# Kernel tuning notes

Hardware: AMD Instinct MI355X
Metric: run time of the kernel (lower is better)

## Reference

```python
import jax, jax.numpy as jnp
import numpy as np

B, N, SD = 2, 128, 3
IN, H, BD, O, L, WF = 16, 128, 32, 12, 2, 4
DEGREE = 2
EPS = 1e-6


def fibonacci_lattice(n, offset=0.5):
    i = jnp.arange(n, dtype=jnp.float32)
    theta = (jnp.pi * i * (1.0 + np.sqrt(5.0))) % (2.0 * jnp.pi)
    phi = jnp.arccos(1.0 - 2.0 * (i + offset) / (n - 1 + 2 * offset))
    return jnp.stack((jnp.sin(phi) * jnp.cos(theta),
                      jnp.sin(phi) * jnp.sin(theta),
                      jnp.cos(phi)), axis=-1)  # (O, 3)


def poly_features(x, degree=DEGREE):
    feats = [x]
    for _ in range(degree):
        new = jnp.einsum('...i,...j->...ij', feats[-1], x).reshape(x.shape[:-1] + (-1,))
        feats.append(new)
    return jnp.concatenate(feats, axis=-1)


def layernorm(x, scale, bias):
    m = x.mean(axis=-1, keepdims=True)
    v = ((x - m) ** 2).mean(axis=-1, keepdims=True)
    return (x - m) * jax.lax.rsqrt(v + EPS) * scale + bias


def _dense(k, fin, fout):
    return jax.random.normal(k, (fin, fout), jnp.float32) / np.sqrt(fin)


def setup_inputs() -> dict:
    key = jax.random.key(0)
    ks = jax.random.split(key, 32)
    SP_IN = 2 + 4 + 8   # poly features of 2-dim spatial invariants, degree 2
    RO_IN = 1 + 1 + 1   # poly features of 1-dim orientation invariant
    inp = {
        'pos': jax.random.normal(ks[0], (B, N, SD), jnp.float32),
        'x': jax.random.normal(ks[1], (B, N, IN), jnp.float32),
        'mask': jnp.ones((B, N), jnp.float32),
        # spatial kernel basis MLP
        'W1s': _dense(ks[2], SP_IN, H), 'b1s': jnp.zeros((H,), jnp.float32),
        'W2s': _dense(ks[3], H, BD),    'b2s': jnp.zeros((BD,), jnp.float32),
        # rotation kernel basis MLP
        'W1r': _dense(ks[4], RO_IN, H), 'b1r': jnp.zeros((H,), jnp.float32),
        'W2r': _dense(ks[5], H, BD),    'b2r': jnp.zeros((BD,), jnp.float32),
        # x embedder (no bias)
        'We': _dense(ks[6], IN, H),
        # per-layer params, stacked along leading layer axis L
        'Wsp':  jax.random.normal(ks[7], (L, BD, H), jnp.float32) / np.sqrt(BD),
        'Wrot': jax.random.normal(ks[8], (L, BD, H), jnp.float32) / np.sqrt(BD),
        'conv_b': jnp.zeros((L, H), jnp.float32),
        'ln_scale': jnp.ones((L, H), jnp.float32),
        'ln_bias': jnp.zeros((L, H), jnp.float32),
        'Wl1': jax.random.normal(ks[9], (L, H, WF * H), jnp.float32) / np.sqrt(H),
        'bl1': jnp.zeros((L, WF * H), jnp.float32),
        'Wl2': jax.random.normal(ks[10], (L, WF * H, H), jnp.float32) / np.sqrt(WF * H),
        'bl2': jnp.zeros((L, H), jnp.float32),
        # readout
        'Wro': _dense(ks[11], H, 1), 'bro': jnp.zeros((1,), jnp.float32),
    }
    return inp


def reference(pos, x, mask, W1s, b1s, W2s, b2s, W1r, b1r, W2r, b2r, We,
              Wsp, Wrot, conv_b, ln_scale, ln_bias, Wl1, bl1, Wl2, bl2, Wro, bro):
    ori = fibonacci_lattice(O)                                   # (O, 3)
    # pairwise relative positions: (B, N_dst=m? note: original indexing)
    rel_pos = pos[:, None, :, None, :] - pos[:, :, None, None, :]  # (B,N,N,1,3)
    inv1 = (rel_pos * ori[None, None, None, :, :]).sum(-1, keepdims=True)        # (B,N,N,O,1)
    inv2 = jnp.linalg.norm(rel_pos - rel_pos * inv1, axis=-1, keepdims=True)     # (B,N,N,O,1)
    spatial_inv = jnp.concatenate([inv1, inv2], axis=-1)          # (B,N,N,O,2)
    ori_inv = (ori[:, None, :] * ori[None, :, :]).sum(-1, keepdims=True)         # (O,O,1)

    gelu = jax.nn.gelu  # approximate tanh gelu, matching flax nn.gelu default
    kernel_basis = gelu(gelu(poly_features(spatial_inv) @ W1s + b1s) @ W2s + b2s)   # (B,N,N,O,BD)
    fiber_basis = gelu(gelu(poly_features(ori_inv) @ W1r + b1r) @ W2r + b2r)        # (O,O,BD)

    h = x @ We                                                    # (B,N,H)
    h = jnp.broadcast_to(h[:, :, None, :], (h.shape[0], h.shape[1], O, h.shape[2]))

    for i in range(L):
        inp = h
        spatial_kernel = kernel_basis @ Wsp[i]                    # (B,N,N,O,H)
        rot_kernel = fiber_basis @ Wrot[i]                        # (O,O,H)
        h = jnp.einsum('bnoc,bmnoc,bn->bmoc', h, spatial_kernel, mask)
        h = jnp.einsum('bmoc,poc->bmpc', h, rot_kernel) / rot_kernel.shape[-2]
        h = h + conv_b[i]
        h = layernorm(h, ln_scale[i], ln_bias[i])
        h = gelu(h @ Wl1[i] + bl1[i]) @ Wl2[i] + bl2[i]
        h = h + inp

    readout = h @ Wro + bro                                       # (B,N,O,1)
    out_scalar = readout.mean(axis=-2)                            # (B,N,1)
    out_scalar = jnp.sum(out_scalar * mask[:, :, None], axis=1) / jnp.sum(mask[:, :, None], axis=1)
    return out_scalar                                             # (B,1)
```

## Files before the change

kernel.cpp:

```cpp
#include <hip/hip_runtime.h>
#include <math.h>

#define NB 2
#define NN 128
#define NO 12
#define NIN 16
#define NH 128
#define NBD 32
#define NL 2
#define NHH 512
#define NSPLIT 8

typedef __attribute__((ext_vector_type(8))) short bf16x8;
typedef __attribute__((ext_vector_type(4))) float f32x4;

__device__ __forceinline__ float gelu_f(float x){
    float x2 = x*x;
    float t = x*(2.3022077f + 0.1029435f*x2);
    float e = __builtin_amdgcn_exp2f(t);
    float r = __builtin_amdgcn_rcpf(e + 1.0f);
    return __builtin_fmaf(-x, r, x);
}

__device__ __forceinline__ ushort f2b(float x){
    union { float f; uint u; } v; v.f = x;
    uint r = v.u + 0x7FFF + ((v.u >> 16) & 1);
    return (ushort)(r >> 16);
}

#define MFMA_BF16(A,B,C) __builtin_amdgcn_mfma_f32_16x16x32_bf16(A,B,C,0,0,0)

__global__ __launch_bounds__(256) void k_setup(const float* __restrict__ W1r,
        const float* __restrict__ b1r, const float* __restrict__ W2r,
        const float* __restrict__ b2r, const float* __restrict__ W1s,
        const float* __restrict__ b1s, const float* __restrict__ W2s,
        const float* __restrict__ Wrot, const float* __restrict__ mask,
        float* __restrict__ ws_ori, float* __restrict__ ws_rot,
        float* __restrict__ ws_rmask,
        ushort* __restrict__ w1ct, ushort* __restrict__ w2ct){
    __shared__ float sori[NO*3];
    __shared__ float sb2r[NBD];
    __shared__ __align__(16) char sWT[8192];
    __shared__ __align__(16) char sHid[160*256];
    __shared__ __align__(16) char sFib[160*64];
    __shared__ __align__(16) char sWrotT[2][8192];

    int tid = threadIdx.x;
    int w = tid >> 6, lane = tid & 63, lr = lane & 15, lg = lane >> 4;

    if (tid < NO){
        float fi = (float)tid;
        float th = fmodf(3.14159265358979323846f * fi * 3.23606797749979f,
                         6.28318530717958647692f);
        float ph = acosf(1.0f - 2.0f*(fi + 0.5f)/12.0f);
        float sp = sinf(ph);
        float ox = sp*cosf(th), oy = sp*sinf(th), oz = cosf(ph);
        sori[tid*3+0]=ox; sori[tid*3+1]=oy; sori[tid*3+2]=oz;
        ws_ori[tid*3+0]=ox; ws_ori[tid*3+1]=oy; ws_ori[tid*3+2]=oz;
    }
    if (tid < NBD) sb2r[tid] = b2r[tid];
    if (tid >= 32 && tid < 32 + NB){
        int b = tid - 32;
        float s = 0.f;
        for (int mm = 0; mm < NN; ++mm) s += mask[b*NN + mm];
        ws_rmask[b] = 1.0f/(12.0f*s);
    }
    if (tid < NH){
        int c = tid;
        float r0 = b1s[c];
        float r1 = W1s[c], r2 = W1s[NH+c], r3 = W1s[2*NH+c];
        float r4 = W1s[3*NH+c] + W1s[4*NH+c];
        float r5 = W1s[5*NH+c], r6 = W1s[6*NH+c];
        float r7 = W1s[7*NH+c] + W1s[8*NH+c] + W1s[10*NH+c];
        float r8 = W1s[9*NH+c] + W1s[11*NH+c] + W1s[12*NH+c];
        float r9 = W1s[13*NH+c];
        ushort* p = w1ct + c*32;
        p[0]=f2b(r0); p[1]=f2b(r1); p[2]=f2b(r2); p[3]=f2b(r3); p[4]=f2b(r4);
        p[5]=f2b(r5); p[6]=f2b(r6); p[7]=f2b(r7); p[8]=f2b(r8); p[9]=f2b(r9);
        #pragma unroll
        for (int k = 10; k < 32; ++k) p[k] = 0;
    }
    for (int e = tid; e < NBD*NH; e += 256){
        int c = e >> 7, k = e & 127;
        w2ct[c*NH + k] = f2b(W2s[k*NBD + c]);
    }
    for (int e = tid; e < NBD*NH; e += 256){
        int c = e >> 7, k = e & 127;
        *(ushort*)(sWT + c*256 + ((k*2) ^ ((c & 7) << 4))) = f2b(W2r[k*NBD + c]);
    }
    for (int e = tid; e < 2*NH*16; e += 256){
        int i = e >> 11, c = (e >> 4) & 127, kk = e & 15;
        const float* wp = Wrot + (size_t)i*NBD*NH + c;
        uint pk = (uint)f2b(wp[(size_t)(2*kk)*NH]) | ((uint)f2b(wp[(size_t)(2*kk+1)*NH]) << 16);
        *(uint*)(sWrotT[i] + c*64 + ((kk*4) ^ ((c & 3) << 4))) = pk;
    }
    for (int e = tid; e < 16*64; e += 256){
        int row = 144 + (e >> 6), k2 = e & 63;
        *(uint*)(sHid + row*256 + ((k2*4) ^ ((row & 7) << 4))) = 0u;
    }
    for (int e = tid; e < 16*16; e += 256){
        int row = 144 + (e >> 4), k2 = e & 15;
        *(uint*)(sFib + row*64 + ((k2*4) ^ ((row & 3) << 4))) = 0u;
    }
    __syncthreads();
    for (int e = tid; e < 144*NH; e += 256){
        int t = e & 127, row = e >> 7;
        int p = row / NO, q = row - (row/NO)*NO;
        float xv = sori[p*3]*sori[q*3] + sori[p*3+1]*sori[q*3+1] + sori[p*3+2]*sori[q*3+2];
        float acc = b1r[t] + xv*(W1r[t] + xv*(W1r[NH+t] + xv*W1r[2*NH+t]));
        *(ushort*)(sHid + row*256 + ((t*2) ^ ((row & 7) << 4))) = f2b(gelu_f(acc));
    }
    __syncthreads();
    for (int tile = w; tile < 5; tile += 4){
        float bv0 = sb2r[lr], bv1 = sb2r[16 + lr];
        f32x4 acc2[2][2];
        acc2[0][0] = (f32x4){bv0,bv0,bv0,bv0}; acc2[0][1] = (f32x4){bv1,bv1,bv1,bv1};
        acc2[1][0] = acc2[0][0]; acc2[1][1] = acc2[0][1];
        #pragma unroll
        for (int kk = 0; kk < 4; ++kk){
            int kbyte = (kk*32 + lg*8)*2;
            int r0 = tile*32 + lr, r1 = r0 + 16;
            bf16x8 a0 = *(const bf16x8*)(sHid + r0*256 + (kbyte ^ ((r0 & 7) << 4)));
            bf16x8 a1 = *(const bf16x8*)(sHid + r1*256 + (kbyte ^ ((r1 & 7) << 4)));
            bf16x8 b0 = *(const bf16x8*)(sWT + lr*256 + (kbyte ^ ((lr & 7) << 4)));
            bf16x8 b1 = *(const bf16x8*)(sWT + (16+lr)*256 + (kbyte ^ ((lr & 7) << 4)));
            acc2[0][0] = MFMA_BF16(a0, b0, acc2[0][0]);
            acc2[0][1] = MFMA_BF16(a0, b1, acc2[0][1]);
            acc2[1][0] = MFMA_BF16(a1, b0, acc2[1][0]);
            acc2[1][1] = MFMA_BF16(a1, b1, acc2[1][1]);
        }
        #pragma unroll
        for (int i = 0; i < 2; ++i)
            #pragma unroll
            for (int j = 0; j < 2; ++j)
                #pragma unroll
                for (int r = 0; r < 4; ++r){
                    int row = tile*32 + i*16 + lg*4 + r, d = j*16 + lr;
                    if (row < 144)
                        *(ushort*)(sFib + row*64 + ((d*2) ^ ((row & 3) << 4)))
                            = f2b(gelu_f(acc2[i][j][r]));
                }
    }
    __syncthreads();
    for (int job = w; job < 20; job += 4){
        int i = job / 10, rt = job - (job/10)*10;
        int rA = rt*16 + lr;
        bf16x8 fa = *(const bf16x8*)(sFib + rA*64 + ((lg*16) ^ ((rA & 3) << 4)));
        #pragma unroll
        for (int j = 0; j < 8; ++j){
            int cB = j*16 + lr;
            bf16x8 fb = *(const bf16x8*)(sWrotT[i] + cB*64 + ((lg*16) ^ ((cB & 3) << 4)));
            f32x4 z = (f32x4){0.f,0.f,0.f,0.f};
            f32x4 acc = MFMA_BF16(fa, fb, z);
            #pragma unroll
            for (int r = 0; r < 4; ++r){
                int row = rt*16 + lg*4 + r;
                if (row < 144)
                    ws_rot[(size_t)i*(144*NH) + (size_t)row*NH + j*16 + lr] = acc[r];
            }
        }
    }
}

__global__ __launch_bounds__(256) void k_embed(const float* __restrict__ x,
        const float* __restrict__ We, float* __restrict__ hE){
    int g = blockIdx.x*256 + threadIdx.x;
    int c = g & 127; int n = (g >> 7) & 127; int b = g >> 14;
    const float* xp = x + ((size_t)b*NN + n)*NIN;
    float acc = 0.f;
    #pragma unroll
    for (int k = 0; k < NIN; ++k) acc += xp[k]*We[k*NH + c];
    hE[g] = acc;
}

__global__ __launch_bounds__(256) void k_kb(const float* __restrict__ pos,
        const ushort* __restrict__ w1ct, const ushort* __restrict__ w2ct,
        const float* __restrict__ b2s, const float* __restrict__ ori,
        ushort* __restrict__ kb){
    __shared__ __align__(16) char smem[49152];
    ushort* sF  = (ushort*)smem;
    char*  sWT  = smem + 8192;
    char*  sH   = smem + 16384;

    int tid = threadIdx.x;
    int bid = blockIdx.x;
    int m = bid & 127; int t2 = bid >> 7;
    int o = t2 % NO, b = t2 / NO;
    int w = tid >> 6, lane = tid & 63, lr = lane & 15, lg = lane >> 4;

    {
        const uint* src = (const uint*)w1ct;
        for (int e = tid; e < 2048; e += 256){
            int c = e >> 4, kk = e & 15;
            *(uint*)(sWT + c*64 + ((kk*4) ^ ((c & 3) << 4))) = src[e];
        }
    }
    if (tid < NN){
        int n = tid;
        float rx = pos[((size_t)b*NN+n)*3+0] - pos[((size_t)b*NN+m)*3+0];
        float ry = pos[((size_t)b*NN+n)*3+1] - pos[((size_t)b*NN+m)*3+1];
        float rz = pos[((size_t)b*NN+n)*3+2] - pos[((size_t)b*NN+m)*3+2];
        float ox = ori[o*3+0], oy = ori[o*3+1], oz = ori[o*3+2];
        float a  = rx*ox + ry*oy + rz*oz;
        float bb = sqrtf(rx*rx+ry*ry+rz*rz) * fabsf(1.0f - a);
        float a2 = a*a, b2 = bb*bb, ab = a*bb;
        float fv[10] = {1.0f, a, bb, a2, ab, b2, a2*a, a2*bb, a*b2, b2*bb};
        char* rowp = (char*)sF + n*64;
        int sw = (n & 3) << 4;
        #pragma unroll
        for (int kk = 0; kk < 5; ++kk){
            uint pk = (uint)f2b(fv[kk*2]) | ((uint)f2b(fv[kk*2+1]) << 16);
            *(uint*)(rowp + ((kk*4) ^ sw)) = pk;
        }
        #pragma unroll
        for (int kk = 5; kk < 16; ++kk)
            *(uint*)(rowp + ((kk*4) ^ sw)) = 0u;
    }
    __syncthreads();
    f32x4 hacc[2][8];
    {
        int rA0 = w*32 + lr, rA1 = rA0 + 16;
        bf16x8 fa0 = *(const bf16x8*)((char*)sF + rA0*64 + ((lg*16) ^ ((rA0 & 3) << 4)));
        bf16x8 fa1 = *(const bf16x8*)((char*)sF + rA1*64 + ((lg*16) ^ ((rA1 & 3) << 4)));
        #pragma unroll
        for (int j = 0; j < 8; ++j){
            int cB = j*16 + lr;
            bf16x8 fb = *(const bf16x8*)(sWT + cB*64 + ((lg*16) ^ ((cB & 3) << 4)));
            f32x4 z = (f32x4){0.f,0.f,0.f,0.f};
            hacc[0][j] = MFMA_BF16(fa0, fb, z);
            hacc[1][j] = MFMA_BF16(fa1, fb, z);
        }
    }
    #pragma unroll
    for (int i = 0; i < 2; ++i)
        #pragma unroll
        for (int j = 0; j < 8; ++j)
            #pragma unroll
            for (int r = 0; r < 4; ++r){
                int n = w*32 + i*16 + lg*4 + r;
                int c = j*16 + lr;
                *(ushort*)(sH + n*256 + ((c*2) ^ ((n & 7) << 4))) = f2b(gelu_f(hacc[i][j][r]));
            }
    __syncthreads();
    {
        const uint* src = (const uint*)w2ct;
        for (int e = tid; e < 2048; e += 256){
            int c = e >> 6, kk = e & 63;
            *(uint*)(sWT + c*256 + ((kk*4) ^ ((c & 7) << 4))) = src[e];
        }
    }
    __syncthreads();
    float bv0 = b2s[lr], bv1 = b2s[16 + lr];
    f32x4 acc2[2][2];
    acc2[0][0] = (f32x4){bv0,bv0,bv0,bv0}; acc2[0][1] = (f32x4){bv1,bv1,bv1,bv1};
    acc2[1][0] = acc2[0][0]; acc2[1][1] = acc2[0][1];
    #pragma unroll
    for (int kk = 0; kk < 4; ++kk){
        int kbyte = (kk*32 + lg*8)*2;
        int r0 = w*32 + lr, r1 = r0 + 16;
        bf16x8 a0 = *(const bf16x8*)(sH + r0*256 + (kbyte ^ ((r0 & 7) << 4)));
        bf16x8 a1 = *(const bf16x8*)(sH + r1*256 + (kbyte ^ ((r1 & 7) << 4)));
        bf16x8 b0 = *(const bf16x8*)(sWT + lr*256 + (kbyte ^ ((lr & 7) << 4)));
        bf16x8 b1 = *(const bf16x8*)(sWT + (16+lr)*256 + (kbyte ^ ((lr & 7) << 4)));
        acc2[0][0] = MFMA_BF16(a0, b0, acc2[0][0]);
        acc2[0][1] = MFMA_BF16(a0, b1, acc2[0][1]);
        acc2[1][0] = MFMA_BF16(a1, b0, acc2[1][0]);
        acc2[1][1] = MFMA_BF16(a1, b1, acc2[1][1]);
    }
    ushort* sOut = (ushort*)smem;
    #pragma unroll
    for (int i = 0; i < 2; ++i)
        #pragma unroll
        for (int j = 0; j < 2; ++j)
            #pragma unroll
            for (int r = 0; r < 4; ++r){
                int n = w*32 + i*16 + lg*4 + r, d = j*16 + lr;
                sOut[n*NBD + d] = f2b(gelu_f(acc2[i][j][r]));
            }
    __syncthreads();
    size_t base = ((size_t)((b*NO + o)*NN + m))*(NN*NBD);
    uint4* dst = (uint4*)(kb + base);
    const uint4* src = (const uint4*)sOut;
    dst[tid] = src[tid];
    dst[256 + tid] = src[256 + tid];
}

__global__ __launch_bounds__(256) void k_convg(const ushort* __restrict__ kb,
        const float* __restrict__ h, const float* __restrict__ wsp_i,
        const float* __restrict__ mask, float* __restrict__ part,
        int sB, int sP){
    __shared__ __align__(16) ushort sA[64*NH];
    __shared__ __align__(16) ushort sW[NH*NH];
    int tid = threadIdx.x;
    int bid = blockIdx.x;
    int s = bid & 7, mh = (bid >> 3) & 1;
    int rest = bid >> 4;
    int o = rest % NO, b = rest / NO;

    int w = tid >> 6, lane = tid & 63, lr = lane & 15, lg = lane >> 4;
    int wm = (w >> 1)*32, wc = (w & 1)*64;

    int c_w = tid & 127, kh = tid >> 7;
    float wv[NBD];
    #pragma unroll
    for (int d = 0; d < NBD; ++d) wv[d] = wsp_i[d*NH + c_w];

    const ushort* abase = kb + ((size_t)(b*NO + o)*NN + mh*64)*(NN*NBD) + s*512;
    const float* hbase = h + (size_t)b*sB + (size_t)o*sP;
    const float* mbase = mask + b*NN;

    f32x4 acc[2][4];
    #pragma unroll
    for (int i = 0; i < 2; ++i)
        #pragma unroll
        for (int j = 0; j < 4; ++j)
            acc[i][j] = (f32x4){0.f,0.f,0.f,0.f};

    for (int ch = 0; ch < 4; ++ch){
        #pragma unroll
        for (int it = 0; it < 4; ++it){
            int flat = it*256 + tid;
            int row = flat >> 4, seg = flat & 15;
            uint4 v = *(const uint4*)(abase + (size_t)row*(NN*NBD) + ch*128 + seg*8);
            *(uint4*)((char*)sA + row*256 + ((seg*16) ^ ((row & 7) << 4))) = v;
        }
        #pragma unroll
        for (int u = 0; u < 2; ++u){
            int n_loc = kh*2 + u;
            int n = s*16 + ch*4 + n_loc;
            float g = hbase[(size_t)n*NH + c_w] * mbase[n];
            #pragma unroll
            for (int q = 0; q < 4; ++q){
                uint4 v;
                v.x = (uint)f2b(g*wv[q*8+0]) | ((uint)f2b(g*wv[q*8+1]) << 16);
                v.y = (uint)f2b(g*wv[q*8+2]) | ((uint)f2b(g*wv[q*8+3]) << 16);
                v.z = (uint)f2b(g*wv[q*8+4]) | ((uint)f2b(g*wv[q*8+5]) << 16);
                v.w = (uint)f2b(g*wv[q*8+6]) | ((uint)f2b(g*wv[q*8+7]) << 16);
                int kbyte = (n_loc*32 + q*8)*2;
                *(uint4*)((char*)sW + c_w*256 + (kbyte ^ ((c_w & 7) << 4))) = v;
            }
        }
        __syncthreads();
        #pragma unroll
        for (int kk = 0; kk < 4; ++kk){
            int kbyte = (kk*32 + lg*8)*2;
            int r0 = wm + lr, r1 = wm + 16 + lr;
            bf16x8 a0 = *(const bf16x8*)((const char*)sA + r0*256 + (kbyte ^ ((r0 & 7) << 4)));
            bf16x8 a1 = *(const bf16x8*)((const char*)sA + r1*256 + (kbyte ^ ((r1 & 7) << 4)));
            bf16x8 bf[4];
            #pragma unroll
            for (int j = 0; j < 4; ++j){
                int c = wc + j*16 + lr;
                bf[j] = *(const bf16x8*)((const char*)sW + c*256 + (kbyte ^ ((c & 7) << 4)));
            }
            #pragma unroll
            for (int j = 0; j < 4; ++j){
                acc[0][j] = MFMA_BF16(a0, bf[j], acc[0][j]);
                acc[1][j] = MFMA_BF16(a1, bf[j], acc[1][j]);
            }
        }
        __syncthreads();
    }
    float* pbase = part + ((size_t)((s*NB + b)*NO + o)*NN + mh*64)*NH;
    #pragma unroll
    for (int i = 0; i < 2; ++i)
        #pragma unroll
        for (int j = 0; j < 4; ++j)
            #pragma unroll
            for (int r = 0; r < 4; ++r){
                int mm = wm + i*16 + lg*4 + r;
                int c = wc + j*16 + lr;
                pbase[(size_t)mm*NH + c] = acc[i][j][r];
            }
}

__global__ __launch_bounds__(512) void k_mlp(const float* __restrict__ part,
        const float* __restrict__ hIn, float* __restrict__ hOut,
        const float* __restrict__ rot_i, const float* __restrict__ convb_i,
        const float* __restrict__ lns_i, const float* __restrict__ lnb_i,
        const float* __restrict__ Wl1_i, const float* __restrict__ bl1_i,
        const float* __restrict__ Wl2_i, const float* __restrict__ bl2_i,
        const float* __restrict__ Wro, const float* __restrict__ bro,
        const float* __restrict__ mask, const float* __restrict__ rmask,
        float* __restrict__ outp, int sB, int sP, int final){
    __shared__ float shcv[NO*NH];
    __shared__ float sy[NO*NH];
    __shared__ float sU[NO*NHH];
    __shared__ float sred[4*NO*NH];
    __shared__ float swred[8];
    int tid = threadIdx.x;
    int bid = blockIdx.x;
    int m = bid & 127, b = bid >> 7;
    for (int e = tid; e < NO*NH; e += 512){
        int o = e >> 7, c = e & 127;
        float sv = 0.f;
        #pragma unroll
        for (int sl = 0; sl < NSPLIT; ++sl)
            sv += part[((size_t)((sl*NB + b)*NO + o)*NN + m)*NH + c];
        shcv[e] = sv;
    }
    __syncthreads();
    for (int e = tid; e < NO*NH; e += 512){
        int p = e >> 7, c = e & 127;
        float acc = 0.f;
        #pragma unroll
        for (int o = 0; o < NO; ++o)
            acc += shcv[o*NH + c]*rot_i[(p*NO + o)*NH + c];
        sy[e] = acc*(1.0f/12.0f) + convb_i[c];
    }
    __syncthreads();
    int wid = tid >> 6, lane = tid & 63;
    for (int row = wid; row < NO; row += 8){
        float x0 = sy[row*NH + lane], x1 = sy[row*NH + 64 + lane];
        float s = x0 + x1, ss = x0*x0 + x1*x1;
        for (int off = 32; off; off >>= 1){
            s  += __shfl_xor(s,  off);
            ss += __shfl_xor(ss, off);
        }
        float mn  = s*(1.0f/128.0f);
        float var = ss*(1.0f/128.0f) - mn*mn;
        float r = rsqrtf(var + 1e-6f);
        sy[row*NH + lane]      = (x0 - mn)*r*lns_i[lane]      + lnb_i[lane];
        sy[row*NH + 64 + lane] = (x1 - mn)*r*lns_i[64 + lane] + lnb_i[64 + lane];
    }
    __syncthreads();
    {
        int j = tid;
        float acc[NO];
        float bj = bl1_i[j];
        #pragma unroll
        for (int p = 0; p < NO; ++p) acc[p] = bj;
        for (int c0 = 0; c0 < NH; c0 += 4){
            f32x4 syv[NO];
            #pragma unroll
            for (int p = 0; p < NO; ++p) syv[p] = *(const f32x4*)&sy[p*NH + c0];
            #pragma unroll
            for (int cc = 0; cc < 4; ++cc){
                float wv = Wl1_i[(size_t)(c0+cc)*NHH + j];
                #pragma unroll
                for (int p = 0; p < NO; ++p) acc[p] += syv[p][cc]*wv;
            }
        }
        #pragma unroll
        for (int p = 0; p < NO; ++p) sU[p*NHH + j] = gelu_f(acc[p]);
    }
    __syncthreads();
    {
        int q = tid >> 7, c = tid & 127;
        float acc[NO];
        #pragma unroll
        for (int p = 0; p < NO; ++p) acc[p] = 0.f;
        for (int j0 = q*128; j0 < q*128 + 128; j0 += 4){
            f32x4 uv[NO];
            #pragma unroll
            for (int p = 0; p < NO; ++p) uv[p] = *(const f32x4*)&sU[p*NHH + j0];
            #pragma unroll
            for (int jj = 0; jj < 4; ++jj){
                float wv = Wl2_i[(size_t)(j0+jj)*NH + c];
                #pragma unroll
                for (int p = 0; p < NO; ++p) acc[p] += uv[p][jj]*wv;
            }
        }
        #pragma unroll
        for (int p = 0; p < NO; ++p) sred[(q*NO + p)*NH + c] = acc[p];
    }
    __syncthreads();
    float ro_part = 0.f;
    for (int e = tid; e < NO*NH; e += 512){
        int p = e >> 7, c = e & 127;
        float v = sred[(0*NO+p)*NH + c] + sred[(1*NO+p)*NH + c]
                + sred[(2*NO+p)*NH + c] + sred[(3*NO+p)*NH + c];
        size_t ri = (size_t)b*sB + (size_t)p*sP + (size_t)m*NH + c;
        float vf = v + bl2_i[c] + hIn[ri];
        if (!final){
            size_t gi = (((size_t)b*NO + p)*NN + m)*NH + c;
            hOut[gi] = vf;
        } else {
            ro_part += vf*Wro[c];
        }
    }
    if (final){
        for (int off = 32; off; off >>= 1) ro_part += __shfl_xor(ro_part, off);
        if (lane == 0) swred[wid] = ro_part;
        __syncthreads();
        if (tid == 0){
            float s = 0.f;
            #pragma unroll
            for (int i = 0; i < 8; ++i) s += swred[i];
            float contrib = (s + 12.0f*bro[0]) * mask[b*NN + m] * rmask[b];
            atomicAdd(&outp[b], contrib);
        }
    }
}

extern "C" void kernel_launch(void* const* d_in, const int* in_sizes, int n_in,
                              void* d_out, int out_size, void* d_ws, size_t ws_size,
                              hipStream_t stream){
    const float* pos  = (const float*)d_in[0];
    const float* x    = (const float*)d_in[1];
    const float* mask = (const float*)d_in[2];
    const float* W1s  = (const float*)d_in[3];
    const float* b1s  = (const float*)d_in[4];
    const float* W2s  = (const float*)d_in[5];
    const float* b2s  = (const float*)d_in[6];
    const float* W1r  = (const float*)d_in[7];
    const float* b1r  = (const float*)d_in[8];
    const float* W2r  = (const float*)d_in[9];
    const float* b2r  = (const float*)d_in[10];
    const float* We   = (const float*)d_in[11];
    const float* Wsp  = (const float*)d_in[12];
    const float* Wrot = (const float*)d_in[13];
    const float* convb= (const float*)d_in[14];
    const float* lns  = (const float*)d_in[15];
    const float* lnb  = (const float*)d_in[16];
    const float* Wl1  = (const float*)d_in[17];
    const float* bl1  = (const float*)d_in[18];
    const float* Wl2  = (const float*)d_in[19];
    const float* bl2  = (const float*)d_in[20];
    const float* Wro  = (const float*)d_in[21];
    const float* bro  = (const float*)d_in[22];

    float* ws = (float*)d_ws;
    float* ws_ori   = ws;
    float* ws_rot   = ws + 64;
    float* ws_rmask = ws + 64 + 36864;
    ushort* w1ct = (ushort*)(ws + 36944);
    ushort* w2ct = (ushort*)(ws + 38992);
    float* hE   = ws + 41040;
    float* hB   = hE + NB*NN*NH;
    float* part = hB + NB*NO*NN*NH;
    ushort* kb  = (ushort*)(part + NSPLIT*NB*NO*NN*NH);

    hipMemsetAsync(d_out, 0, (size_t)out_size*sizeof(float), stream);

    k_setup<<<1, 256, 0, stream>>>(W1r, b1r, W2r, b2r, W1s, b1s, W2s,
                                   Wrot, mask, ws_ori, ws_rot, ws_rmask,
                                   w1ct, w2ct);
    k_embed<<<NB*NN*NH/256, 256, 0, stream>>>(x, We, hE);
    k_kb<<<NB*NO*NN, 256, 0, stream>>>(pos, w1ct, w2ct, b2s, ws_ori, kb);

    k_convg<<<NB*NO*2*NSPLIT, 256, 0, stream>>>(kb, hE, Wsp, mask, part,
            NN*NH, 0);
    k_mlp<<<NB*NN, 512, 0, stream>>>(part, hE, hB,
            ws_rot, convb, lns, lnb, Wl1, bl1, Wl2, bl2,
            Wro, bro, mask, ws_rmask, (float*)d_out, NN*NH, 0, 0);
    k_convg<<<NB*NO*2*NSPLIT, 256, 0, stream>>>(kb, hB, Wsp + NBD*NH, mask, part,
            NO*NN*NH, NN*NH);
    k_mlp<<<NB*NN, 512, 0, stream>>>(part, hB, hB,
            ws_rot + 144*NH, convb + NH, lns + NH, lnb + NH,
            Wl1 + NH*NHH, bl1 + NHH, Wl2 + NHH*NH, bl2 + NH,
            Wro, bro, mask, ws_rmask, (float*)d_out, NO*NN*NH, NN*NH, 1);
}
```

Measured before the change: 261.2 us.

## Reduce split-K conv partials with atomics and widen MLP block to 1024 threads

```diff
diff --git a/kernel.cpp b/kernel.cpp
--- a/kernel.cpp
+++ b/kernel.cpp
@@ -287,7 +287,7 @@
 
 __global__ __launch_bounds__(256) void k_convg(const ushort* __restrict__ kb,
         const float* __restrict__ h, const float* __restrict__ wsp_i,
-        const float* __restrict__ mask, float* __restrict__ part,
+        const float* __restrict__ mask, float* __restrict__ hconv,
         int sB, int sP){
     __shared__ __align__(16) ushort sA[64*NH];
     __shared__ __align__(16) ushort sW[NH*NH];
@@ -361,7 +361,7 @@
         }
         __syncthreads();
     }
-    float* pbase = part + ((size_t)((s*NB + b)*NO + o)*NN + mh*64)*NH;
+    float* obase = hconv + ((size_t)(b*NO + o)*NN + mh*64)*NH;
     #pragma unroll
     for (int i = 0; i < 2; ++i)
         #pragma unroll
@@ -370,11 +370,11 @@
             for (int r = 0; r < 4; ++r){
                 int mm = wm + i*16 + lg*4 + r;
                 int c = wc + j*16 + lr;
-                pbase[(size_t)mm*NH + c] = acc[i][j][r];
-            }
-}
-
-__global__ __launch_bounds__(512) void k_mlp(const float* __restrict__ part,
+                atomicAdd(&obase[(size_t)mm*NH + c], acc[i][j][r]);
+            }
+}
+
+__global__ __launch_bounds__(1024) void k_mlp(const float* __restrict__ hconv,
         const float* __restrict__ hIn, float* __restrict__ hOut,
         const float* __restrict__ rot_i, const float* __restrict__ convb_i,
         const float* __restrict__ lns_i, const float* __restrict__ lnb_i,
@@ -387,30 +387,33 @@
     __shared__ float sy[NO*NH];
     __shared__ float sU[NO*NHH];
     __shared__ float sred[4*NO*NH];
-    __shared__ float swred[8];
+    __shared__ float swred[16];
     int tid = threadIdx.x;
     int bid = blockIdx.x;
     int m = bid & 127, b = bid >> 7;
-    for (int e = tid; e < NO*NH; e += 512){
-        int o = e >> 7, c = e & 127;
-        float sv = 0.f;
-        #pragma unroll
-        for (int sl = 0; sl < NSPLIT; ++sl)
-            sv += part[((size_t)((sl*NB + b)*NO + o)*NN + m)*NH + c];
-        shcv[e] = sv;
-    }
-    __syncthreads();
-    for (int e = tid; e < NO*NH; e += 512){
-        int p = e >> 7, c = e & 127;
-        float acc = 0.f;
-        #pragma unroll
-        for (int o = 0; o < NO; ++o)
-            acc += shcv[o*NH + c]*rot_i[(p*NO + o)*NH + c];
-        sy[e] = acc*(1.0f/12.0f) + convb_i[c];
-    }
-    __syncthreads();
     int wid = tid >> 6, lane = tid & 63;
-    for (int row = wid; row < NO; row += 8){
+
+    if (tid < NO*NH/4){
+        int o = tid >> 5, c4 = tid & 31;
+        ((f32x4*)shcv)[tid] =
+            ((const f32x4*)hconv)[((size_t)(b*NO + o)*NN + m)*(NH/4) + c4];
+    }
+    __syncthreads();
+    if (tid < NO*NH/4){
+        int p = tid >> 5, c4 = tid & 31;
+        f32x4 acc = (f32x4){0.f,0.f,0.f,0.f};
+        #pragma unroll
+        for (int o = 0; o < NO; ++o){
+            f32x4 hv = ((const f32x4*)shcv)[o*(NH/4) + c4];
+            f32x4 rv = ((const f32x4*)rot_i)[(p*NO + o)*(NH/4) + c4];
+            acc += hv*rv;
+        }
+        f32x4 cb = ((const f32x4*)convb_i)[c4];
+        ((f32x4*)sy)[tid] = acc*(1.0f/12.0f) + cb;
+    }
+    __syncthreads();
+    if (wid < NO){
+        int row = wid;
         float x0 = sy[row*NH + lane], x1 = sy[row*NH + 64 + lane];
         float s = x0 + x1, ss = x0*x0 + x1*x1;
         for (int off = 32; off; off >>= 1){
@@ -425,24 +428,26 @@
     }
     __syncthreads();
     {
-        int j = tid;
-        float acc[NO];
+        int j = tid & 511, ph = tid >> 9;
+        int p0 = ph*6;
+        float acc[6];
         float bj = bl1_i[j];
         #pragma unroll
-        for (int p = 0; p < NO; ++p) acc[p] = bj;
+        for (int p = 0; p < 6; ++p) acc[p] = bj;
         for (int c0 = 0; c0 < NH; c0 += 4){
-            f32x4 syv[NO];
-            #pragma unroll
-            for (int p = 0; p < NO; ++p) syv[p] = *(const f32x4*)&sy[p*NH + c0];
+            f32x4 syv[6];
+            #pragma unroll
+            for (int p = 0; p < 6; ++p)
+                syv[p] = *(const f32x4*)&sy[(p0 + p)*NH + c0];
             #pragma unroll
             for (int cc = 0; cc < 4; ++cc){
                 float wv = Wl1_i[(size_t)(c0+cc)*NHH + j];
                 #pragma unroll
-                for (int p = 0; p < NO; ++p) acc[p] += syv[p][cc]*wv;
-            }
-        }
-        #pragma unroll
-        for (int p = 0; p < NO; ++p) sU[p*NHH + j] = gelu_f(acc[p]);
+                for (int p = 0; p < 6; ++p) acc[p] += syv[p][cc]*wv;
+            }
+        }
+        #pragma unroll
+        for (int p = 0; p < 6; ++p) sU[(p0 + p)*NHH + j] = gelu_f(acc[p]);
     }
     __syncthreads();
     {
@@ -450,7 +455,7 @@
         float acc[NO];
         #pragma unroll
         for (int p = 0; p < NO; ++p) acc[p] = 0.f;
-        for (int j0 = q*128; j0 < q*128 + 128; j0 += 4){
+        for (int j0 = q*64; j0 < q*64 + 64; j0 += 4){
             f32x4 uv[NO];
             #pragma unroll
             for (int p = 0; p < NO; ++p) uv[p] = *(const f32x4*)&sU[p*NHH + j0];
@@ -461,22 +466,34 @@
                 for (int p = 0; p < NO; ++p) acc[p] += uv[p][jj]*wv;
             }
         }
-        #pragma unroll
-        for (int p = 0; p < NO; ++p) sred[(q*NO + p)*NH + c] = acc[p];
+        if (q >= 4){
+            #pragma unroll
+            for (int p = 0; p < NO; ++p) sred[((q-4)*NO + p)*NH + c] = acc[p];
+        }
+        __syncthreads();
+        if (q < 4){
+            #pragma unroll
+            for (int p = 0; p < NO; ++p) sred[(q*NO + p)*NH + c] += acc[p];
+        }
     }
     __syncthreads();
     float ro_part = 0.f;
-    for (int e = tid; e < NO*NH; e += 512){
-        int p = e >> 7, c = e & 127;
-        float v = sred[(0*NO+p)*NH + c] + sred[(1*NO+p)*NH + c]
-                + sred[(2*NO+p)*NH + c] + sred[(3*NO+p)*NH + c];
-        size_t ri = (size_t)b*sB + (size_t)p*sP + (size_t)m*NH + c;
-        float vf = v + bl2_i[c] + hIn[ri];
+    if (tid < NO*NH/4){
+        int p = tid >> 5, c4 = tid & 31;
+        f32x4 v = ((const f32x4*)sred)[(0*NO + p)*(NH/4) + c4]
+                + ((const f32x4*)sred)[(1*NO + p)*(NH/4) + c4]
+                + ((const f32x4*)sred)[(2*NO + p)*(NH/4) + c4]
+                + ((const f32x4*)sred)[(3*NO + p)*(NH/4) + c4];
+        f32x4 bv = ((const f32x4*)bl2_i)[c4];
+        size_t ri4 = ((size_t)b*sB + (size_t)p*sP + (size_t)m*NH)/4 + c4;
+        f32x4 hv = ((const f32x4*)hIn)[ri4];
+        f32x4 vf = v + bv + hv;
         if (!final){
-            size_t gi = (((size_t)b*NO + p)*NN + m)*NH + c;
-            hOut[gi] = vf;
+            size_t gi4 = (((size_t)b*NO + p)*NN + m)*(NH/4) + c4;
+            ((f32x4*)hOut)[gi4] = vf;
         } else {
-            ro_part += vf*Wro[c];
+            f32x4 wr = ((const f32x4*)Wro)[c4];
+            ro_part = vf.x*wr.x + vf.y*wr.y + vf.z*wr.z + vf.w*wr.w;
         }
     }
     if (final){
@@ -486,7 +503,7 @@
         if (tid == 0){
             float s = 0.f;
             #pragma unroll
-            for (int i = 0; i < 8; ++i) s += swred[i];
+            for (int i = 0; i < 16; ++i) s += swred[i];
             float contrib = (s + 12.0f*bro[0]) * mask[b*NN + m] * rmask[b];
             atomicAdd(&outp[b], contrib);
         }
@@ -526,10 +543,10 @@
     float* ws_rmask = ws + 64 + 36864;
     ushort* w1ct = (ushort*)(ws + 36944);
     ushort* w2ct = (ushort*)(ws + 38992);
-    float* hE   = ws + 41040;
-    float* hB   = hE + NB*NN*NH;
-    float* part = hB + NB*NO*NN*NH;
-    ushort* kb  = (ushort*)(part + NSPLIT*NB*NO*NN*NH);
+    float* hE    = ws + 41040;
+    float* hB    = hE + NB*NN*NH;
+    float* hconv = hB + NB*NO*NN*NH;
+    ushort* kb   = (ushort*)(hconv + NB*NO*NN*NH);
 
     hipMemsetAsync(d_out, 0, (size_t)out_size*sizeof(float), stream);
 
@@ -539,14 +556,16 @@
     k_embed<<<NB*NN*NH/256, 256, 0, stream>>>(x, We, hE);
     k_kb<<<NB*NO*NN, 256, 0, stream>>>(pos, w1ct, w2ct, b2s, ws_ori, kb);
 
-    k_convg<<<NB*NO*2*NSPLIT, 256, 0, stream>>>(kb, hE, Wsp, mask, part,
+    hipMemsetAsync(hconv, 0, (size_t)NB*NO*NN*NH*sizeof(float), stream);
+    k_convg<<<NB*NO*2*NSPLIT, 256, 0, stream>>>(kb, hE, Wsp, mask, hconv,
             NN*NH, 0);
-    k_mlp<<<NB*NN, 512, 0, stream>>>(part, hE, hB,
+    k_mlp<<<NB*NN, 1024, 0, stream>>>(hconv, hE, hB,
             ws_rot, convb, lns, lnb, Wl1, bl1, Wl2, bl2,
             Wro, bro, mask, ws_rmask, (float*)d_out, NN*NH, 0, 0);
-    k_convg<<<NB*NO*2*NSPLIT, 256, 0, stream>>>(kb, hB, Wsp + NBD*NH, mask, part,
+    hipMemsetAsync(hconv, 0, (size_t)NB*NO*NN*NH*sizeof(float), stream);
+    k_convg<<<NB*NO*2*NSPLIT, 256, 0, stream>>>(kb, hB, Wsp + NBD*NH, mask, hconv,
             NO*NN*NH, NN*NH);
-    k_mlp<<<NB*NN, 512, 0, stream>>>(part, hB, hB,
+    k_mlp<<<NB*NN, 1024, 0, stream>>>(hconv, hB, hB,
             ws_rot + 144*NH, convb + NH, lns + NH, lnb + NH,
             Wl1 + NH*NHH, bl1 + NHH, Wl2 + NHH*NH, bl2 + NH,
             Wro, bro, mask, ws_rmask, (float*)d_out, NO*NN*NH, NN*NH, 1);
```

Result: no change. 258.1 us (-1.2%).
